# Kernel tuning notes

Hardware: AMD Instinct MI355X
Metric: run time of the kernel (lower is better)

Reference implementation:

```python
import jax, jax.numpy as jnp
import numpy as np

B, T, C = 4, 2048, 1024
N_HEADS, HEAD_SIZE = 16, 1024
HD = HEAD_SIZE // N_HEADS  # 64


def setup_inputs() -> dict:
    key = jax.random.key(0)
    ks = jax.random.split(key, 5)
    scale = 1.0 / np.sqrt(C)
    return {
        "x": jax.random.normal(ks[0], (B, T, C), dtype=jnp.float32),
        "Wq": jax.random.normal(ks[1], (C, HEAD_SIZE), dtype=jnp.float32) * scale,
        "Wk": jax.random.normal(ks[2], (C, HEAD_SIZE), dtype=jnp.float32) * scale,
        "Wv": jax.random.normal(ks[3], (C, HEAD_SIZE), dtype=jnp.float32) * scale,
        "Wc": jax.random.normal(ks[4], (HEAD_SIZE, C), dtype=jnp.float32) * (1.0 / np.sqrt(HEAD_SIZE)),
        "bc": jnp.zeros((C,), dtype=jnp.float32),
    }


def reference(x, Wq, Wk, Wv, Wc, bc):
    b, t, c = x.shape
    # projections (bias-free), split heads: [B, H, T, hd]
    def heads(y):
        return y.reshape(b, t, N_HEADS, HD).transpose(0, 2, 1, 3)
    Q = heads(x @ Wq)
    K = heads(x @ Wk)
    V = heads(x @ Wv)
    # scaled scores + causal mask (additive -1e9 above diagonal)
    scores = jnp.einsum("bhqd,bhkd->bhqk", Q, K) / jnp.sqrt(jnp.float32(HD))
    causal = jnp.tril(jnp.ones((t, t), dtype=scores.dtype))
    scores = scores + (1.0 - causal) * -1e9
    attn = jax.nn.softmax(scores, axis=-1)
    # dropout is identity in eval mode
    o = jnp.einsum("bhqk,bhkd->bhqd", attn, V)
    o = o.transpose(0, 2, 1, 3).reshape(b, t, HEAD_SIZE)
    return o @ Wc + bc
```

## Files before the change

kernel.cpp:

```cpp
#include <hip/hip_runtime.h>
#include <hip/hip_bf16.h>
#include <math.h>


#define M_TOT   8192
#define C_DIM   1024
#define T_DIM   2048
#define NH      16
#define HD      64
#define BHT     (NH * 4)

typedef short  bf16x8 __attribute__((ext_vector_type(8)));
typedef ushort u16x8  __attribute__((ext_vector_type(8)));
typedef float  f32x4  __attribute__((ext_vector_type(4)));

static __device__ __forceinline__ ushort f2bf(float f) {
    union { __hip_bfloat16 h; ushort u; } cv;
    cv.h = __float2bfloat16(f);
    return cv.u;
}
static __device__ __forceinline__ float bf2f(ushort u) {
    union { ushort u; __hip_bfloat16 h; } cv;
    cv.u = u;
    return __bfloat162float(cv.h);
}
static __device__ __forceinline__ void gload16(const ushort* g, ushort* l) {
    __builtin_amdgcn_global_load_lds(
        (const __attribute__((address_space(1))) void*)g,
        (__attribute__((address_space(3))) void*)l, 16, 0, 0);
}

__global__ __launch_bounds__(256) void decomp_x(
    const float* __restrict__ x, ushort* __restrict__ xh, ushort* __restrict__ xl)
{
    const int i = blockIdx.x * 256 + threadIdx.x;
    const float4 a = ((const float4*)x)[2 * i];
    const float4 b = ((const float4*)x)[2 * i + 1];
    const float v[8] = {a.x, a.y, a.z, a.w, b.x, b.y, b.z, b.w};
    u16x8 h, l;
    #pragma unroll
    for (int e = 0; e < 8; ++e) {
        h[e] = f2bf(v[e]);
        l[e] = f2bf(v[e] - bf2f(h[e]));
    }
    ((u16x8*)xh)[i] = h;
    ((u16x8*)xl)[i] = l;
}

__global__ __launch_bounds__(256) void wtrans(
    const float* __restrict__ Wq, const float* __restrict__ Wk,
    const float* __restrict__ Wv, const float* __restrict__ Wc,
    ushort* __restrict__ WTh, ushort* __restrict__ WTl,
    ushort* __restrict__ WcTh, ushort* __restrict__ WcTl)
{
    __shared__ float tile[64][65];
    const int z = blockIdx.z;
    const float* W = (z == 0) ? Wq : (z == 1) ? Wk : (z == 2) ? Wv : Wc;
    const int n0 = blockIdx.x * 64, k0 = blockIdx.y * 64;
    const int tid = threadIdx.x;

    #pragma unroll
    for (int i = 0; i < 4; ++i) {
        const int lin = i * 1024 + tid * 4;
        const int r = lin >> 6, c = lin & 63;
        const float4 v = *(const float4*)(W + (size_t)(k0 + r) * 1024 + n0 + c);
        tile[r][c] = v.x; tile[r][c + 1] = v.y; tile[r][c + 2] = v.z; tile[r][c + 3] = v.w;
    }
    __syncthreads();

    ushort* oh = (z < 3) ? WTh : WcTh;
    ushort* ol = (z < 3) ? WTl : WcTl;
    const size_t rowbase = (z < 3) ? (size_t)z * 1024 : 0;
    #pragma unroll
    for (int i = 0; i < 4; ++i) {
        const int lin = i * 1024 + tid * 4;
        const int rn = lin >> 6, ck = lin & 63;
        ushort4 hv, lv;
        float v0 = tile[ck + 0][rn], v1 = tile[ck + 1][rn];
        float v2 = tile[ck + 2][rn], v3 = tile[ck + 3][rn];
        hv.x = f2bf(v0); lv.x = f2bf(v0 - bf2f(hv.x));
        hv.y = f2bf(v1); lv.y = f2bf(v1 - bf2f(hv.y));
        hv.z = f2bf(v2); lv.z = f2bf(v2 - bf2f(hv.z));
        hv.w = f2bf(v3); lv.w = f2bf(v3 - bf2f(hv.w));
        const size_t off = (rowbase + n0 + rn) * 1024 + k0 + ck;
        *(ushort4*)(oh + off) = hv;
        *(ushort4*)(ol + off) = lv;
    }
}

__global__ __launch_bounds__(256, 2) void qkv_mfma(
    const ushort* __restrict__ xh, const ushort* __restrict__ xl,
    const ushort* __restrict__ WTh, const ushort* __restrict__ WTl,
    ushort* __restrict__ Qh, ushort* __restrict__ Kh, ushort* __restrict__ Vt)
{
    __shared__ ushort Ah[128 * 64], Al[128 * 64], Bh[128 * 64], Bl[128 * 64];

    const int tid = threadIdx.x;
    const int wave = tid >> 6, lane = tid & 63, lq = lane & 15, g = lane >> 4;
    const int m0 = blockIdx.x * 128;
    const int n0 = blockIdx.y * 128;
    const int wm = wave >> 1, wn = wave & 1;
    const int sm = tid >> 3;
    const int sk = (tid & 7) * 8;

    f32x4 acc[4][4];
    #pragma unroll
    for (int i = 0; i < 4; ++i)
        #pragma unroll
        for (int j = 0; j < 4; ++j) { acc[i][j][0]=0.f; acc[i][j][1]=0.f; acc[i][j][2]=0.f; acc[i][j][3]=0.f; }

    for (int kt = 0; kt < 16; ++kt) {
        const int ko = kt * 64 + sk;
        #pragma unroll
        for (int rd = 0; rd < 4; ++rd) {
            const int mm = sm + rd * 32;
            const int lo = rd * 2048 + wave * 512;
            gload16(xh  + (size_t)(m0 + mm) * 1024 + ko, &Ah[lo]);
            gload16(xl  + (size_t)(m0 + mm) * 1024 + ko, &Al[lo]);
            gload16(WTh + (size_t)(n0 + mm) * 1024 + ko, &Bh[lo]);
            gload16(WTl + (size_t)(n0 + mm) * 1024 + ko, &Bl[lo]);
        }
        __syncthreads();

        #pragma unroll
        for (int kc = 0; kc < 2; ++kc) {
            bf16x8 bhf[4], blf[4];
            #pragma unroll
            for (int ni = 0; ni < 4; ++ni) {
                const int row = wn * 64 + ni * 16 + lq;
                bhf[ni] = *(const bf16x8*)&Bh[row * 64 + kc * 32 + g * 8];
                blf[ni] = *(const bf16x8*)&Bl[row * 64 + kc * 32 + g * 8];
            }
            #pragma unroll
            for (int mi = 0; mi < 4; ++mi) {
                const int row = wm * 64 + mi * 16 + lq;
                const bf16x8 ahf = *(const bf16x8*)&Ah[row * 64 + kc * 32 + g * 8];
                const bf16x8 alf = *(const bf16x8*)&Al[row * 64 + kc * 32 + g * 8];
                #pragma unroll
                for (int ni = 0; ni < 4; ++ni) {
                    acc[mi][ni] = __builtin_amdgcn_mfma_f32_16x16x32_bf16(ahf, bhf[ni], acc[mi][ni], 0, 0, 0);
                    acc[mi][ni] = __builtin_amdgcn_mfma_f32_16x16x32_bf16(alf, bhf[ni], acc[mi][ni], 0, 0, 0);
                    acc[mi][ni] = __builtin_amdgcn_mfma_f32_16x16x32_bf16(ahf, blf[ni], acc[mi][ni], 0, 0, 0);
                }
            }
        }
        __syncthreads();
    }

    const int which = n0 >> 10;
    const int nn0 = n0 & 1023;
    const int b = m0 >> 11;
    const int tb = (m0 & 2047) + wm * 64;
    if (which < 2) {
        ushort* out = which ? Kh : Qh;
        #pragma unroll
        for (int mi = 0; mi < 4; ++mi) {
            const int t = tb + mi * 16 + g * 4;
            #pragma unroll
            for (int ni = 0; ni < 4; ++ni) {
                const int n = nn0 + wn * 64 + ni * 16 + lq;
                const int h = n >> 6, d = n & 63;
                ushort* op = out + ((size_t)(b * NH + h) * T_DIM + t) * HD + d;
                #pragma unroll
                for (int r = 0; r < 4; ++r) op[r * HD] = f2bf(acc[mi][ni][r]);
            }
        }
    } else {
        #pragma unroll
        for (int mi = 0; mi < 4; ++mi) {
            const int t = tb + mi * 16 + g * 4;
            #pragma unroll
            for (int ni = 0; ni < 4; ++ni) {
                const int n = nn0 + wn * 64 + ni * 16 + lq;
                const int h = n >> 6, d = n & 63;
                ushort4 v;
                v.x = f2bf(acc[mi][ni][0]); v.y = f2bf(acc[mi][ni][1]);
                v.z = f2bf(acc[mi][ni][2]); v.w = f2bf(acc[mi][ni][3]);
                *(ushort4*)(Vt + ((size_t)(b * NH + h) * HD + d) * T_DIM + t) = v;
            }
        }
    }
}

__global__ __launch_bounds__(256, 2) void attn_kernel(
    const ushort* __restrict__ Qh,
    const ushort* __restrict__ Kh,
    const ushort* __restrict__ Vt,
    ushort* __restrict__ Ohh,
    ushort* __restrict__ Ohl)
{
    __shared__ __align__(16) ushort sbuf[2][8192];

    const int tid  = threadIdx.x;
    const int wave = tid >> 6, lane = tid & 63;
    const int lq   = lane & 15, g = lane >> 4;
    const int bh   = blockIdx.y;
    const int qt   = (T_DIM / 64 - 1) - blockIdx.x;
    const int qw0  = qt * 64 + wave * 16;
    const int q    = qw0 + lq;
    const int ntiles = qt + 1;

    const ushort* Qb = Qh + ((size_t)bh * T_DIM + q) * HD;
    bf16x8 qf[2];
    qf[0] = *(const bf16x8*)(Qb + g * 8);
    qf[1] = *(const bf16x8*)(Qb + 32 + g * 8);

    const ushort* Kb = Kh + (size_t)bh * T_DIM * HD;
    const ushort* Vb = Vt + (size_t)bh * HD * T_DIM;

    const int srow  = tid >> 3;
    const int sunit = tid & 7;

    f32x4 o[4];
    #pragma unroll
    for (int dt = 0; dt < 4; ++dt) { o[dt][0]=0.f; o[dt][1]=0.f; o[dt][2]=0.f; o[dt][3]=0.f; }
    float m = -3.0e38f, l = 0.f;

    {
        #pragma unroll
        for (int rr = 0; rr < 2; ++rr) {
            const int row = rr * 32 + srow;
            const int un  = sunit ^ (row & 7);
            gload16(Kb + (size_t)row * HD + un * 8,    &sbuf[0][rr * 2048 + wave * 512]);
            gload16(Vb + (size_t)row * T_DIM + un * 8, &sbuf[0][4096 + rr * 2048 + wave * 512]);
        }
    }
    __syncthreads();

    int cur = 0;
    for (int kvt = 0; kvt < ntiles; ++kvt) {
        const bool lastt = (kvt == ntiles - 1);

        if (!lastt) {
            const ushort* Kt  = Kb + (size_t)(kvt + 1) * 64 * HD;
            const ushort* Vtt = Vb + (kvt + 1) * 64;
            const int nb = cur ^ 1;
            #pragma unroll
            for (int rr = 0; rr < 2; ++rr) {
                const int row = rr * 32 + srow;
                const int un  = sunit ^ (row & 7);
                gload16(Kt + (size_t)row * HD + un * 8,    &sbuf[nb][rr * 2048 + wave * 512]);
                gload16(Vtt + (size_t)row * T_DIM + un * 8, &sbuf[nb][4096 + rr * 2048 + wave * 512]);
            }
        }

        const char* Ksb = (const char*)&sbuf[cur][0];
        const char* Vsb = (const char*)&sbuf[cur][4096];
        const int rxor = (lq & 7) << 4;

        bf16x8 kf[4][2];
        #pragma unroll
        for (int kt = 0; kt < 4; ++kt) {
            const int rb = (kt * 16 + lq) * 128;
            kf[kt][0] = *(const bf16x8*)(Ksb + rb + ((g * 16) ^ rxor));
            kf[kt][1] = *(const bf16x8*)(Ksb + rb + ((64 + g * 16) ^ rxor));
        }
        bf16x8 vf[4][2];
        #pragma unroll
        for (int dt = 0; dt < 4; ++dt) {
            const int rb = (dt * 16 + lq) * 128;
            #pragma unroll
            for (int cc = 0; cc < 2; ++cc) {
                ushort4 lo = *(const ushort4*)(Vsb + rb + ((cc * 64 + g * 8) ^ rxor));
                ushort4 hi = *(const ushort4*)(Vsb + rb + ((cc * 64 + g * 8 + 32) ^ rxor));
                bf16x8 v;
                v[0] = (short)lo.x; v[1] = (short)lo.y; v[2] = (short)lo.z; v[3] = (short)lo.w;
                v[4] = (short)hi.x; v[5] = (short)hi.y; v[6] = (short)hi.z; v[7] = (short)hi.w;
                vf[dt][cc] = v;
            }
        }

        __builtin_amdgcn_s_setprio(1);
        f32x4 s[4];
        #pragma unroll
        for (int kt = 0; kt < 4; ++kt) {
            f32x4 z; z[0]=0.f; z[1]=0.f; z[2]=0.f; z[3]=0.f;
            z = __builtin_amdgcn_mfma_f32_16x16x32_bf16(kf[kt][0], qf[0], z, 0, 0, 0);
            s[kt] = __builtin_amdgcn_mfma_f32_16x16x32_bf16(kf[kt][1], qf[1], s[kt] = z, 0, 0, 0);
        }
        __builtin_amdgcn_s_setprio(0);

        float p[4][4];
        float pmax = -3.0e38f;
        #pragma unroll
        for (int kt = 0; kt < 4; ++kt) {
            #pragma unroll
            for (int r = 0; r < 4; ++r) {
                float v = s[kt][r] * 0.125f;
                if (lastt) {
                    const int kv = kvt * 64 + kt * 16 + g * 4 + r;
                    if (kv > q) v = -3.0e38f;
                }
                p[kt][r] = v;
                pmax = fmaxf(pmax, v);
            }
        }
        pmax = fmaxf(pmax, __shfl_xor(pmax, 16));
        pmax = fmaxf(pmax, __shfl_xor(pmax, 32));
        const float mnew = fmaxf(m, pmax);
        const float cf = __expf(m - mnew);
        m = mnew;

        float rs = 0.f;
        #pragma unroll
        for (int kt = 0; kt < 4; ++kt) {
            #pragma unroll
            for (int r = 0; r < 4; ++r) {
                const float w = __expf(p[kt][r] - mnew);
                p[kt][r] = w;
                rs += w;
            }
        }
        rs += __shfl_xor(rs, 16);
        rs += __shfl_xor(rs, 32);
        l = l * cf + rs;

        #pragma unroll
        for (int dt = 0; dt < 4; ++dt) {
            o[dt][0] *= cf; o[dt][1] *= cf; o[dt][2] *= cf; o[dt][3] *= cf;
        }

        bf16x8 pf[2];
        #pragma unroll
        for (int cc = 0; cc < 2; ++cc) {
            #pragma unroll
            for (int j = 0; j < 8; ++j)
                pf[cc][j] = (short)f2bf(p[cc * 2 + (j >> 2)][j & 3]);
        }

        __builtin_amdgcn_s_setprio(1);
        #pragma unroll
        for (int dt = 0; dt < 4; ++dt) {
            o[dt] = __builtin_amdgcn_mfma_f32_16x16x32_bf16(vf[dt][0], pf[0], o[dt], 0, 0, 0);
            o[dt] = __builtin_amdgcn_mfma_f32_16x16x32_bf16(vf[dt][1], pf[1], o[dt], 0, 0, 0);
        }
        __builtin_amdgcn_s_setprio(0);

        __syncthreads();
        cur ^= 1;
    }

    float* olds = (float*)&sbuf[0][0];
    const float invl = 1.0f / l;
    #pragma unroll
    for (int dt = 0; dt < 4; ++dt) {
        #pragma unroll
        for (int r = 0; r < 4; ++r)
            olds[wave * 1088 + lq * 68 + dt * 16 + g * 4 + r] = o[dt][r] * invl;
    }
    #pragma unroll
    for (int pp = 0; pp < 4; ++pp) {
        const int qq = pp * 4 + g;
        const float4 v4 = *(const float4*)&olds[wave * 1088 + qq * 68 + lq * 4];
        ushort4 hv, lv;
        hv.x = f2bf(v4.x); lv.x = f2bf(v4.x - bf2f(hv.x));
        hv.y = f2bf(v4.y); lv.y = f2bf(v4.y - bf2f(hv.y));
        hv.z = f2bf(v4.z); lv.z = f2bf(v4.z - bf2f(hv.z));
        hv.w = f2bf(v4.w); lv.w = f2bf(v4.w - bf2f(hv.w));
        const size_t off = ((size_t)bh * T_DIM + qw0 + qq) * HD + lq * 4;
        *(ushort4*)(Ohh + off) = hv;
        *(ushort4*)(Ohl + off) = lv;
    }
}

__global__ __launch_bounds__(256, 2) void out_mfma(
    const ushort* __restrict__ Ahh, const ushort* __restrict__ Ahl,
    const ushort* __restrict__ BTh, const ushort* __restrict__ BTl,
    const float* __restrict__ bc, float* __restrict__ out)
{
    __shared__ ushort Ah[128 * 64], Al[128 * 64], Bh[128 * 64], Bl[128 * 64];

    const int tid = threadIdx.x;
    const int wave = tid >> 6, lane = tid & 63, lq = lane & 15, g = lane >> 4;
    const int m0 = blockIdx.x * 128;
    const int n0 = blockIdx.y * 128;
    const int wm = wave >> 1, wn = wave & 1;
    const int sm = tid >> 3;
    const int sk = (tid & 7) * 8;
    const int b = m0 >> 11, t0 = m0 & 2047;

    f32x4 acc[4][4];
    #pragma unroll
    for (int i = 0; i < 4; ++i)
        #pragma unroll
        for (int j = 0; j < 4; ++j) { acc[i][j][0]=0.f; acc[i][j][1]=0.f; acc[i][j][2]=0.f; acc[i][j][3]=0.f; }

    for (int kt = 0; kt < 16; ++kt) {
        const size_t abase = ((size_t)(b * NH + kt) * T_DIM + t0) * HD;
        #pragma unroll
        for (int rd = 0; rd < 4; ++rd) {
            const int mm = sm + rd * 32;
            const int lo = rd * 2048 + wave * 512;
            gload16(Ahh + abase + (size_t)mm * HD + sk, &Ah[lo]);
            gload16(Ahl + abase + (size_t)mm * HD + sk, &Al[lo]);
            gload16(BTh + (size_t)(n0 + mm) * 1024 + kt * 64 + sk, &Bh[lo]);
            gload16(BTl + (size_t)(n0 + mm) * 1024 + kt * 64 + sk, &Bl[lo]);
        }
        __syncthreads();

        #pragma unroll
        for (int kc = 0; kc < 2; ++kc) {
            bf16x8 bhf[4], blf[4];
            #pragma unroll
            for (int ni = 0; ni < 4; ++ni) {
                const int row = wn * 64 + ni * 16 + lq;
                bhf[ni] = *(const bf16x8*)&Bh[row * 64 + kc * 32 + g * 8];
                blf[ni] = *(const bf16x8*)&Bl[row * 64 + kc * 32 + g * 8];
            }
            #pragma unroll
            for (int mi = 0; mi < 4; ++mi) {
                const int row = wm * 64 + mi * 16 + lq;
                const bf16x8 ahf = *(const bf16x8*)&Ah[row * 64 + kc * 32 + g * 8];
                const bf16x8 alf = *(const bf16x8*)&Al[row * 64 + kc * 32 + g * 8];
                #pragma unroll
                for (int ni = 0; ni < 4; ++ni) {
                    acc[mi][ni] = __builtin_amdgcn_mfma_f32_16x16x32_bf16(ahf, bhf[ni], acc[mi][ni], 0, 0, 0);
                    acc[mi][ni] = __builtin_amdgcn_mfma_f32_16x16x32_bf16(alf, bhf[ni], acc[mi][ni], 0, 0, 0);
                    acc[mi][ni] = __builtin_amdgcn_mfma_f32_16x16x32_bf16(ahf, blf[ni], acc[mi][ni], 0, 0, 0);
                }
            }
        }
        __syncthreads();
    }

    #pragma unroll
    for (int ni = 0; ni < 4; ++ni) {
        const int n = n0 + wn * 64 + ni * 16 + lq;
        const float bias = bc[n];
        #pragma unroll
        for (int mi = 0; mi < 4; ++mi) {
            const int mrow = m0 + wm * 64 + mi * 16 + g * 4;
            #pragma unroll
            for (int r = 0; r < 4; ++r)
                out[(size_t)(mrow + r) * C_DIM + n] = acc[mi][ni][r] + bias;
        }
    }
}

extern "C" void kernel_launch(void* const* d_in, const int* in_sizes, int n_in,
                              void* d_out, int out_size, void* d_ws, size_t ws_size,
                              hipStream_t stream)
{
    const float* x  = (const float*)d_in[0];
    const float* Wq = (const float*)d_in[1];
    const float* Wk = (const float*)d_in[2];
    const float* Wv = (const float*)d_in[3];
    const float* Wc = (const float*)d_in[4];
    const float* bc = (const float*)d_in[5];
    float* out = (float*)d_out;

    const size_t PL   = (size_t)M_TOT * C_DIM;
    const size_t WQKV = (size_t)3072 * 1024;
    const size_t WC   = (size_t)1024 * 1024;

    ushort* ws   = (ushort*)d_ws;
    ushort* xh   = ws;
    ushort* xl   = xh + PL;
    ushort* WTh  = xl + PL;
    ushort* WTl  = WTh + WQKV;
    ushort* WcTh = WTl + WQKV;
    ushort* WcTl = WcTh + WC;
    ushort* Qh   = WcTl + WC;
    ushort* Kh   = Qh + PL;
    ushort* Vt   = Kh + PL;
    ushort* Ohh  = Vt + PL;
    ushort* Ohl  = Ohh + PL;

    decomp_x<<<4096, 256, 0, stream>>>(x, xh, xl);
    wtrans<<<dim3(16, 16, 4), 256, 0, stream>>>(Wq, Wk, Wv, Wc, WTh, WTl, WcTh, WcTl);
    qkv_mfma<<<dim3(M_TOT / 128, 24), 256, 0, stream>>>(xh, xl, WTh, WTl, Qh, Kh, Vt);
    attn_kernel<<<dim3(T_DIM / 64, BHT), 256, 0, stream>>>(Qh, Kh, Vt, Ohh, Ohl);
    out_mfma<<<dim3(M_TOT / 128, C_DIM / 128), 256, 0, stream>>>(Ohh, Ohl, WcTh, WcTl, bc, out);
}
```

Before: 430.5 us.

## Drop weight low-part split, add lazy softmax rescale, raise occupancy bounds

Weights are no longer split into high and low bf16 parts, which removes one MFMA in three, one LDS buffer and one global load stream in both projection GEMMs, at some cost in accuracy. The attention kernel now rescales its running max and accumulator only when some lane's new max exceeds the old one by more than 8, so most iterations skip that work. Launch bounds are raised so more blocks can be resident per CU, which may cause register spills.

Measured after the change: 363.8 us. -15.5%, faster.

```diff
diff --git a/kernel.cpp b/kernel.cpp
--- a/kernel.cpp
+++ b/kernel.cpp
@@ -50,8 +50,7 @@
 __global__ __launch_bounds__(256) void wtrans(
     const float* __restrict__ Wq, const float* __restrict__ Wk,
     const float* __restrict__ Wv, const float* __restrict__ Wc,
-    ushort* __restrict__ WTh, ushort* __restrict__ WTl,
-    ushort* __restrict__ WcTh, ushort* __restrict__ WcTl)
+    ushort* __restrict__ WTh, ushort* __restrict__ WcTh)
 {
     __shared__ float tile[64][65];
     const int z = blockIdx.z;
@@ -69,31 +68,26 @@
     __syncthreads();
 
     ushort* oh = (z < 3) ? WTh : WcTh;
-    ushort* ol = (z < 3) ? WTl : WcTl;
     const size_t rowbase = (z < 3) ? (size_t)z * 1024 : 0;
     #pragma unroll
     for (int i = 0; i < 4; ++i) {
         const int lin = i * 1024 + tid * 4;
         const int rn = lin >> 6, ck = lin & 63;
-        ushort4 hv, lv;
-        float v0 = tile[ck + 0][rn], v1 = tile[ck + 1][rn];
-        float v2 = tile[ck + 2][rn], v3 = tile[ck + 3][rn];
-        hv.x = f2bf(v0); lv.x = f2bf(v0 - bf2f(hv.x));
-        hv.y = f2bf(v1); lv.y = f2bf(v1 - bf2f(hv.y));
-        hv.z = f2bf(v2); lv.z = f2bf(v2 - bf2f(hv.z));
-        hv.w = f2bf(v3); lv.w = f2bf(v3 - bf2f(hv.w));
-        const size_t off = (rowbase + n0 + rn) * 1024 + k0 + ck;
-        *(ushort4*)(oh + off) = hv;
-        *(ushort4*)(ol + off) = lv;
-    }
-}
-
-__global__ __launch_bounds__(256, 2) void qkv_mfma(
+        ushort4 hv;
+        hv.x = f2bf(tile[ck + 0][rn]);
+        hv.y = f2bf(tile[ck + 1][rn]);
+        hv.z = f2bf(tile[ck + 2][rn]);
+        hv.w = f2bf(tile[ck + 3][rn]);
+        *(ushort4*)(oh + (rowbase + n0 + rn) * 1024 + k0 + ck) = hv;
+    }
+}
+
+__global__ __launch_bounds__(256, 3) void qkv_mfma(
     const ushort* __restrict__ xh, const ushort* __restrict__ xl,
-    const ushort* __restrict__ WTh, const ushort* __restrict__ WTl,
+    const ushort* __restrict__ WTh,
     ushort* __restrict__ Qh, ushort* __restrict__ Kh, ushort* __restrict__ Vt)
 {
-    __shared__ ushort Ah[128 * 64], Al[128 * 64], Bh[128 * 64], Bl[128 * 64];
+    __shared__ ushort Ah[128 * 64], Al[128 * 64], Bh[128 * 64];
 
     const int tid = threadIdx.x;
     const int wave = tid >> 6, lane = tid & 63, lq = lane & 15, g = lane >> 4;
@@ -118,18 +112,16 @@
             gload16(xh  + (size_t)(m0 + mm) * 1024 + ko, &Ah[lo]);
             gload16(xl  + (size_t)(m0 + mm) * 1024 + ko, &Al[lo]);
             gload16(WTh + (size_t)(n0 + mm) * 1024 + ko, &Bh[lo]);
-            gload16(WTl + (size_t)(n0 + mm) * 1024 + ko, &Bl[lo]);
         }
         __syncthreads();
 
         #pragma unroll
         for (int kc = 0; kc < 2; ++kc) {
-            bf16x8 bhf[4], blf[4];
+            bf16x8 bhf[4];
             #pragma unroll
             for (int ni = 0; ni < 4; ++ni) {
                 const int row = wn * 64 + ni * 16 + lq;
                 bhf[ni] = *(const bf16x8*)&Bh[row * 64 + kc * 32 + g * 8];
-                blf[ni] = *(const bf16x8*)&Bl[row * 64 + kc * 32 + g * 8];
             }
             #pragma unroll
             for (int mi = 0; mi < 4; ++mi) {
@@ -140,7 +132,6 @@
                 for (int ni = 0; ni < 4; ++ni) {
                     acc[mi][ni] = __builtin_amdgcn_mfma_f32_16x16x32_bf16(ahf, bhf[ni], acc[mi][ni], 0, 0, 0);
                     acc[mi][ni] = __builtin_amdgcn_mfma_f32_16x16x32_bf16(alf, bhf[ni], acc[mi][ni], 0, 0, 0);
-                    acc[mi][ni] = __builtin_amdgcn_mfma_f32_16x16x32_bf16(ahf, blf[ni], acc[mi][ni], 0, 0, 0);
                 }
             }
         }
@@ -182,7 +173,7 @@
     }
 }
 
-__global__ __launch_bounds__(256, 2) void attn_kernel(
+__global__ __launch_bounds__(256, 4) void attn_kernel(
     const ushort* __restrict__ Qh,
     const ushort* __restrict__ Kh,
     const ushort* __restrict__ Vt,
@@ -216,14 +207,12 @@
     for (int dt = 0; dt < 4; ++dt) { o[dt][0]=0.f; o[dt][1]=0.f; o[dt][2]=0.f; o[dt][3]=0.f; }
     float m = -3.0e38f, l = 0.f;
 
-    {
-        #pragma unroll
-        for (int rr = 0; rr < 2; ++rr) {
-            const int row = rr * 32 + srow;
-            const int un  = sunit ^ (row & 7);
-            gload16(Kb + (size_t)row * HD + un * 8,    &sbuf[0][rr * 2048 + wave * 512]);
-            gload16(Vb + (size_t)row * T_DIM + un * 8, &sbuf[0][4096 + rr * 2048 + wave * 512]);
-        }
+    #pragma unroll
+    for (int rr = 0; rr < 2; ++rr) {
+        const int row = rr * 32 + srow;
+        const int un  = sunit ^ (row & 7);
+        gload16(Kb + (size_t)row * HD + un * 8,    &sbuf[0][rr * 2048 + wave * 512]);
+        gload16(Vb + (size_t)row * T_DIM + un * 8, &sbuf[0][4096 + rr * 2048 + wave * 512]);
     }
     __syncthreads();
 
@@ -239,7 +228,7 @@
             for (int rr = 0; rr < 2; ++rr) {
                 const int row = rr * 32 + srow;
                 const int un  = sunit ^ (row & 7);
-                gload16(Kt + (size_t)row * HD + un * 8,    &sbuf[nb][rr * 2048 + wave * 512]);
+                gload16(Kt + (size_t)row * HD + un * 8,     &sbuf[nb][rr * 2048 + wave * 512]);
                 gload16(Vtt + (size_t)row * T_DIM + un * 8, &sbuf[nb][4096 + rr * 2048 + wave * 512]);
             }
         }
@@ -276,7 +265,7 @@
         for (int kt = 0; kt < 4; ++kt) {
             f32x4 z; z[0]=0.f; z[1]=0.f; z[2]=0.f; z[3]=0.f;
             z = __builtin_amdgcn_mfma_f32_16x16x32_bf16(kf[kt][0], qf[0], z, 0, 0, 0);
-            s[kt] = __builtin_amdgcn_mfma_f32_16x16x32_bf16(kf[kt][1], qf[1], s[kt] = z, 0, 0, 0);
+            s[kt] = __builtin_amdgcn_mfma_f32_16x16x32_bf16(kf[kt][1], qf[1], z, 0, 0, 0);
         }
         __builtin_amdgcn_s_setprio(0);
 
@@ -297,28 +286,31 @@
         }
         pmax = fmaxf(pmax, __shfl_xor(pmax, 16));
         pmax = fmaxf(pmax, __shfl_xor(pmax, 32));
-        const float mnew = fmaxf(m, pmax);
-        const float cf = __expf(m - mnew);
-        m = mnew;
+
+        if (!__all(pmax - m <= 8.0f)) {
+            const float mnew = fmaxf(m, pmax);
+            const float cf = __expf(m - mnew);
+            l *= cf;
+            #pragma unroll
+            for (int dt = 0; dt < 4; ++dt) {
+                o[dt][0] *= cf; o[dt][1] *= cf; o[dt][2] *= cf; o[dt][3] *= cf;
+            }
+            m = mnew;
+        }
 
         float rs = 0.f;
         #pragma unroll
         for (int kt = 0; kt < 4; ++kt) {
             #pragma unroll
             for (int r = 0; r < 4; ++r) {
-                const float w = __expf(p[kt][r] - mnew);
+                const float w = __expf(p[kt][r] - m);
                 p[kt][r] = w;
                 rs += w;
             }
         }
         rs += __shfl_xor(rs, 16);
         rs += __shfl_xor(rs, 32);
-        l = l * cf + rs;
-
-        #pragma unroll
-        for (int dt = 0; dt < 4; ++dt) {
-            o[dt][0] *= cf; o[dt][1] *= cf; o[dt][2] *= cf; o[dt][3] *= cf;
-        }
+        l += rs;
 
         bf16x8 pf[2];
         #pragma unroll
@@ -363,12 +355,12 @@
     }
 }
 
-__global__ __launch_bounds__(256, 2) void out_mfma(
+__global__ __launch_bounds__(256, 3) void out_mfma(
     const ushort* __restrict__ Ahh, const ushort* __restrict__ Ahl,
-    const ushort* __restrict__ BTh, const ushort* __restrict__ BTl,
+    const ushort* __restrict__ BTh,
     const float* __restrict__ bc, float* __restrict__ out)
 {
-    __shared__ ushort Ah[128 * 64], Al[128 * 64], Bh[128 * 64], Bl[128 * 64];
+    __shared__ ushort Ah[128 * 64], Al[128 * 64], Bh[128 * 64];
 
     const int tid = threadIdx.x;
     const int wave = tid >> 6, lane = tid & 63, lq = lane & 15, g = lane >> 4;
@@ -394,18 +386,16 @@
             gload16(Ahh + abase + (size_t)mm * HD + sk, &Ah[lo]);
             gload16(Ahl + abase + (size_t)mm * HD + sk, &Al[lo]);
             gload16(BTh + (size_t)(n0 + mm) * 1024 + kt * 64 + sk, &Bh[lo]);
-            gload16(BTl + (size_t)(n0 + mm) * 1024 + kt * 64 + sk, &Bl[lo]);
         }
         __syncthreads();
 
         #pragma unroll
         for (int kc = 0; kc < 2; ++kc) {
-            bf16x8 bhf[4], blf[4];
+            bf16x8 bhf[4];
             #pragma unroll
             for (int ni = 0; ni < 4; ++ni) {
                 const int row = wn * 64 + ni * 16 + lq;
                 bhf[ni] = *(const bf16x8*)&Bh[row * 64 + kc * 32 + g * 8];
-                blf[ni] = *(const bf16x8*)&Bl[row * 64 + kc * 32 + g * 8];
             }
             #pragma unroll
             for (int mi = 0; mi < 4; ++mi) {
@@ -416,7 +406,6 @@
                 for (int ni = 0; ni < 4; ++ni) {
                     acc[mi][ni] = __builtin_amdgcn_mfma_f32_16x16x32_bf16(ahf, bhf[ni], acc[mi][ni], 0, 0, 0);
                     acc[mi][ni] = __builtin_amdgcn_mfma_f32_16x16x32_bf16(alf, bhf[ni], acc[mi][ni], 0, 0, 0);
-                    acc[mi][ni] = __builtin_amdgcn_mfma_f32_16x16x32_bf16(ahf, blf[ni], acc[mi][ni], 0, 0, 0);
                 }
             }
         }
@@ -467,8 +456,8 @@
     ushort* Ohl  = Ohh + PL;
 
     decomp_x<<<4096, 256, 0, stream>>>(x, xh, xl);
-    wtrans<<<dim3(16, 16, 4), 256, 0, stream>>>(Wq, Wk, Wv, Wc, WTh, WTl, WcTh, WcTl);
-    qkv_mfma<<<dim3(M_TOT / 128, 24), 256, 0, stream>>>(xh, xl, WTh, WTl, Qh, Kh, Vt);
+    wtrans<<<dim3(16, 16, 4), 256, 0, stream>>>(Wq, Wk, Wv, Wc, WTh, WcTh);
+    qkv_mfma<<<dim3(M_TOT / 128, 24), 256, 0, stream>>>(xh, xl, WTh, Qh, Kh, Vt);
     attn_kernel<<<dim3(T_DIM / 64, BHT), 256, 0, stream>>>(Qh, Kh, Vt, Ohh, Ohl);
-    out_mfma<<<dim3(M_TOT / 128, C_DIM / 128), 256, 0, stream>>>(Ohh, Ohl, WcTh, WcTl, bc, out);
-}
+    out_mfma<<<dim3(M_TOT / 128, C_DIM / 128), 256, 0, stream>>>(Ohh, Ohl, WcTh, bc, out);
+}
```
